# Kernel optimization log

Hardware: AMD Instinct MI355X
Metric: run time of the kernel (lower is better)

## Reference

```python
import jax, jax.numpy as jnp
import numpy as np

N = 25000      # nodes
E = 400000     # edges
IN = 1024      # in_channels
FC = 128       # feature_channels
ADD = 20       # additional_channels
MID = (FC + ADD) // 4   # 37, fc1 output (heads=4)
OUT = 3
EPS = 1e-5
NEG_SLOPE = 0.01


def setup_inputs() -> dict:
    key = jax.random.key(0)
    ks = jax.random.split(key, 16)
    d = {}
    d["features"] = jax.random.normal(ks[0], (N, IN), dtype=jnp.float32)
    d["edges"] = jax.random.randint(ks[1], (2, E), 0, N, dtype=jnp.int64)
    d["edges2"] = jax.random.randint(ks[2], (2, 1000), 0, N, dtype=jnp.int64)
    d["edge_features"] = jax.random.normal(ks[3], (E, 1), dtype=jnp.float32)
    d["additional_feature"] = jax.random.normal(ks[4], (N, ADD), dtype=jnp.float32)
    # SAGEConv params: lin_l (neighbor path, with bias), lin_r (root path, no bias)
    s = 1.0 / np.sqrt(IN)
    d["Wl"] = jax.random.uniform(ks[5], (FC, IN), jnp.float32, -s, s)
    d["bl"] = jax.random.uniform(ks[6], (FC,), jnp.float32, -s, s)
    d["Wr"] = jax.random.uniform(ks[7], (FC, IN), jnp.float32, -s, s)
    s1 = 1.0 / np.sqrt(FC + ADD)
    d["W1"] = jax.random.uniform(ks[8], (MID, FC + ADD), jnp.float32, -s1, s1)
    d["b1"] = jax.random.uniform(ks[9], (MID,), jnp.float32, -s1, s1)
    s2 = 1.0 / np.sqrt(MID)
    d["W2"] = jax.random.uniform(ks[10], (OUT, MID), jnp.float32, -s2, s2)
    d["b2"] = jax.random.uniform(ks[11], (OUT,), jnp.float32, -s2, s2)
    # BatchNorm1d (eval mode -> running stats)
    d["gamma"] = jnp.ones((MID,), jnp.float32)
    d["beta"] = jnp.zeros((MID,), jnp.float32)
    d["run_mean"] = jax.random.normal(ks[12], (MID,), dtype=jnp.float32) * 0.1
    d["run_var"] = jnp.abs(jax.random.normal(ks[13], (MID,), dtype=jnp.float32)) * 0.1 + 1.0
    return d


def reference(features, edges, edges2, edge_features, additional_feature,
              Wl, bl, Wr, W1, b1, W2, b2, gamma, beta, run_mean, run_var):
    src, dst = edges[0], edges[1]  # PyG: messages flow source -> target
    # scatter-mean of neighbor features onto targets
    agg = jax.ops.segment_sum(features[src], dst, num_segments=N)        # [N, IN]
    deg = jax.ops.segment_sum(jnp.ones((E,), features.dtype), dst, num_segments=N)
    agg = agg / jnp.maximum(deg, 1.0)[:, None]
    # SAGEConv: lin_l(mean_neigh) + lin_r(x)
    x = agg @ Wl.T + bl + features @ Wr.T                                 # [N, FC]
    x = jnp.where(x >= 0, x, NEG_SLOPE * x)                               # leaky_relu
    # dropout is identity in eval mode
    x = jnp.concatenate([x, additional_feature], axis=1) @ W1.T + b1      # [N, MID]
    x = jnp.maximum(x, 0.0)                                               # relu
    x = gamma * (x - run_mean) * jax.lax.rsqrt(run_var + EPS) + beta      # BN eval
    return x @ W2.T + b2                                                  # [N, OUT]
```

## Files before the change

### kernel.cpp

```cpp
#include <hip/hip_runtime.h>

#define N_NODES 25000
#define N_EDGES 400000
#define IN_CH 1024
#define FC 128
#define ADD_CH 20
#define XCH 148
#define MID 37
#define OUT_CH 3
#define MAXDEG 64

typedef short bf16x8 __attribute__((ext_vector_type(8)));
typedef float f32x4 __attribute__((ext_vector_type(4)));

__device__ __forceinline__ float bflo(unsigned int v) {
    return __builtin_bit_cast(float, v << 16);
}
__device__ __forceinline__ float bfhi(unsigned int v) {
    return __builtin_bit_cast(float, v & 0xffff0000u);
}
__device__ __forceinline__ unsigned int cvtpk(float a, float b) {
    unsigned int r;
    asm("v_cvt_pk_bf16_f32 %0, %1, %2" : "=v"(r) : "v"(a), "v"(b));
    return r;
}

__device__ __forceinline__ void gload16(const void* g, void* l) {
    __builtin_amdgcn_global_load_lds(
        (const __attribute__((address_space(1))) unsigned int*)g,
        (__attribute__((address_space(3))) unsigned int*)l,
        16, 0, 0);
}

#define WSWZ_B 16
#define ZERO_B 49

__global__ __launch_bounds__(512) void prep(const float* __restrict__ Wl,
                                            const float* __restrict__ Wr,
                                            ushort* __restrict__ Wpk,
                                            int* __restrict__ cursor) {
    int b = blockIdx.x, t = threadIdx.x;
    if (b < WSWZ_B) {
        int w = t >> 6, lane = t & 63, l15 = lane & 15, q8 = (lane >> 4) * 8;
        int ch = b * 16 + l15;
        const float* src = (ch < FC) ? (Wl + (size_t)ch * IN_CH)
                                     : (Wr + (size_t)(ch - FC) * IN_CH);
        #pragma unroll
        for (int j = 0; j < 4; ++j) {
            int kt = w * 4 + j;
            float4 lo = *(const float4*)(src + kt * 32 + q8);
            float4 hi = *(const float4*)(src + kt * 32 + q8 + 4);
            uint4 pk;
            pk.x = cvtpk(lo.x, lo.y); pk.y = cvtpk(lo.z, lo.w);
            pk.z = cvtpk(hi.x, hi.y); pk.w = cvtpk(hi.z, hi.w);
            ((uint4*)Wpk)[((size_t)kt * 16 + b) * 64 + lane] = pk;
        }
    } else {
        int i = (b - WSWZ_B) * 512 + t;
        if (i < N_NODES) cursor[i] = 0;
    }
}

#define GEMM_B 391
#define BUILD_B 782

__global__ __launch_bounds__(512, 4) void gemm_build(const float* __restrict__ A,
                                                     const ushort* __restrict__ Wpk,
                                                     ushort* __restrict__ Py,
                                                     ushort* __restrict__ Pz,
                                                     const int* __restrict__ edges,
                                                     int* __restrict__ cursor,
                                                     int* __restrict__ col) {
    __shared__ uint4 LDS[2][1536];
    int b = blockIdx.x, t = threadIdx.x;
    if (b >= GEMM_B) {
        int e = (b - GEMM_B) * 512 + t;
        if (e < N_EDGES) {
            int dst = edges[N_EDGES + e];
            int pos = atomicAdd(&cursor[dst], 1);
            if (pos < MAXDEG) col[dst * MAXDEG + pos] = edges[e];
        }
        return;
    }
    int m0 = b * 64;

    int ga = t >> 7, hq = (t >> 6) & 1, la = t & 63;
    int nodeA = m0 + ga * 16 + (la & 15);
    if (nodeA >= N_NODES) nodeA = N_NODES - 1;
    const float* Asrc = A + (size_t)nodeA * IN_CH + (la >> 4) * 8 + hq * 4;
    const uint4* Wg = (const uint4*)Wpk;
    int tb = t & ~63;

    int w = t >> 6, lane = t & 63;
    int wm = w >> 2, wn = w & 3;
    int l15 = lane & 15, q = lane >> 4;

    f32x4 acc[4][2] = {};

    gload16(Wg + t,       &LDS[0][tb]);
    gload16(Wg + 512 + t, &LDS[0][512 + tb]);
    gload16(Asrc,         &LDS[0][1024 + tb]);
    __syncthreads();

    for (int c = 0; c < 32; ++c) {
        int cur = c & 1;
        if (c + 1 < 32) {
            const uint4* ws = Wg + (size_t)(c + 1) * 1024;
            gload16(ws + t,       &LDS[cur ^ 1][tb]);
            gload16(ws + 512 + t, &LDS[cur ^ 1][512 + tb]);
            gload16(Asrc + (size_t)(c + 1) * 32, &LDS[cur ^ 1][1024 + tb]);
        }
        bf16x8 wf[4];
        #pragma unroll
        for (int i = 0; i < 4; ++i)
            wf[i] = *(const bf16x8*)&LDS[cur][(wn * 4 + i) * 64 + lane];
        bf16x8 af[2];
        #pragma unroll
        for (int g2 = 0; g2 < 2; ++g2) {
            f32x4 lo = *(const f32x4*)&LDS[cur][1024 + ((wm * 2 + g2) * 2 + 0) * 64 + lane];
            f32x4 hi = *(const f32x4*)&LDS[cur][1024 + ((wm * 2 + g2) * 2 + 1) * 64 + lane];
            uint4 pk;
            pk.x = cvtpk(lo[0], lo[1]); pk.y = cvtpk(lo[2], lo[3]);
            pk.z = cvtpk(hi[0], hi[1]); pk.w = cvtpk(hi[2], hi[3]);
            af[g2] = __builtin_bit_cast(bf16x8, pk);
        }
        #pragma unroll
        for (int i = 0; i < 4; ++i)
            #pragma unroll
            for (int g2 = 0; g2 < 2; ++g2)
                acc[i][g2] = __builtin_amdgcn_mfma_f32_16x16x32_bf16(wf[i], af[g2], acc[i][g2], 0, 0, 0);
        __syncthreads();
    }

    #pragma unroll
    for (int g2 = 0; g2 < 2; ++g2) {
        int node = m0 + wm * 32 + g2 * 16 + l15;
        if (node < N_NODES) {
            ushort* base = (wn < 2) ? (Py + (size_t)node * FC + (wn & 1) * 64 + q * 4)
                                    : (Pz + (size_t)node * FC + (wn & 1) * 64 + q * 4);
            #pragma unroll
            for (int i = 0; i < 4; ++i) {
                f32x4 v = acc[i][g2];
                uint2 pk;
                pk.x = cvtpk(v[0], v[1]);
                pk.y = cvtpk(v[2], v[3]);
                *(uint2*)(base + i * 16) = pk;
            }
        }
    }
}

__global__ __launch_bounds__(512) void fused_tail(const ushort* __restrict__ Py,
                                                  const ushort* __restrict__ Pz,
                                                  const int* __restrict__ deg,
                                                  const int* __restrict__ col,
                                                  const float* __restrict__ addf,
                                                  const float* __restrict__ bl,
                                                  const float* __restrict__ W1,
                                                  const float* __restrict__ b1,
                                                  const float* __restrict__ W2,
                                                  const float* __restrict__ b2,
                                                  const float* __restrict__ gamma,
                                                  const float* __restrict__ beta,
                                                  const float* __restrict__ rmean,
                                                  const float* __restrict__ rvar,
                                                  float* __restrict__ out) {
    __shared__ float W1s[XCH][MID + 3];
    __shared__ float xbuf[8][XCH + 4];
    __shared__ float hbuf[8][MID + 3];
    int t = threadIdx.x;
    for (int idx = t; idx < MID * XCH; idx += 512) {
        int j = idx / XCH, k = idx - j * XCH;
        W1s[k][j] = W1[idx];
    }
    __syncthreads();
    int w = t >> 6, lane = t & 63;
    int n = blockIdx.x * 8 + w;
    bool valid = (n < N_NODES);
    int d = valid ? deg[n] : 0;
    if (d > MAXDEG) d = MAXDEG;
    int g = lane >> 4, c16 = lane & 15;
    float s[8] = {0.f, 0.f, 0.f, 0.f, 0.f, 0.f, 0.f, 0.f};
    if (d > 0) {
        int cidx = col[n * MAXDEG + (lane < d ? lane : 0)];
        for (int i = 0; i < d; i += 16) {
            int e[4];
            uint4 v[4];
            #pragma unroll
            for (int j = 0; j < 4; ++j) {
                int ee = i + g + j * 4;
                e[j] = __shfl(cidx, (ee < d) ? ee : 0);
            }
            #pragma unroll
            for (int j = 0; j < 4; ++j)
                v[j] = *(const uint4*)&Py[(size_t)e[j] * FC + c16 * 8];
            #pragma unroll
            for (int j = 0; j < 4; ++j) {
                if (i + g + j * 4 < d) {
                    s[0] += bflo(v[j].x); s[1] += bfhi(v[j].x);
                    s[2] += bflo(v[j].y); s[3] += bfhi(v[j].y);
                    s[4] += bflo(v[j].z); s[5] += bfhi(v[j].z);
                    s[6] += bflo(v[j].w); s[7] += bfhi(v[j].w);
                }
            }
        }
        #pragma unroll
        for (int r = 0; r < 8; ++r) {
            s[r] += __shfl_xor(s[r], 16);
            s[r] += __shfl_xor(s[r], 32);
        }
    }
    if (valid) {
        if (lane < 16) {
            #pragma unroll
            for (int r = 0; r < 8; ++r) xbuf[w][lane * 8 + r] = s[r];
        }
        float invd = 1.0f / (float)(d > 1 ? d : 1);
        unsigned int vr = *(const unsigned int*)&Pz[(size_t)n * FC + lane * 2];
        float x0 = xbuf[w][2 * lane] * invd + bl[2 * lane] + bflo(vr);
        float x1 = xbuf[w][2 * lane + 1] * invd + bl[2 * lane + 1] + bfhi(vr);
        x0 = (x0 >= 0.f) ? x0 : 0.01f * x0;
        x1 = (x1 >= 0.f) ? x1 : 0.01f * x1;
        xbuf[w][2 * lane] = x0;
        xbuf[w][2 * lane + 1] = x1;
        if (lane < ADD_CH) xbuf[w][FC + lane] = addf[(size_t)n * ADD_CH + lane];
        if (lane < MID) {
            float h = b1[lane];
            #pragma unroll 4
            for (int k = 0; k < XCH; ++k) h += W1s[k][lane] * xbuf[w][k];
            h = fmaxf(h, 0.0f);
            h = gamma[lane] * (h - rmean[lane]) * rsqrtf(rvar[lane] + 1e-5f) + beta[lane];
            hbuf[w][lane] = h;
        }
        if (lane < OUT_CH) {
            float o = b2[lane];
            #pragma unroll
            for (int j = 0; j < MID; ++j) o += W2[lane * MID + j] * hbuf[w][j];
            out[(size_t)n * OUT_CH + lane] = o;
        }
    }
}


extern "C" void kernel_launch(void* const* d_in, const int* in_sizes, int n_in,
                              void* d_out, int out_size, void* d_ws, size_t ws_size,
                              hipStream_t stream) {
    const float* features = (const float*)d_in[0];
    const int*   edges    = (const int*)d_in[1];
    const float* addf     = (const float*)d_in[4];
    const float* Wl       = (const float*)d_in[5];
    const float* bl       = (const float*)d_in[6];
    const float* Wr       = (const float*)d_in[7];
    const float* W1       = (const float*)d_in[8];
    const float* b1       = (const float*)d_in[9];
    const float* W2       = (const float*)d_in[10];
    const float* b2       = (const float*)d_in[11];
    const float* gamma    = (const float*)d_in[12];
    const float* beta     = (const float*)d_in[13];
    const float* rmean    = (const float*)d_in[14];
    const float* rvar     = (const float*)d_in[15];
    float* out = (float*)d_out;

    char* ws = (char*)d_ws;
    size_t off = 0;
    ushort* Py = (ushort*)(ws + off);     off += (size_t)N_NODES * FC * 2;
    ushort* Pz = (ushort*)(ws + off);     off += (size_t)N_NODES * FC * 2;
    ushort* Wpk = (ushort*)(ws + off);    off += (size_t)32 * 16 * 64 * 16;
    int* cursor = (int*)(ws + off);       off += (size_t)N_NODES * 4;
    int* col = (int*)(ws + off);          off += (size_t)N_NODES * MAXDEG * 4;

    prep<<<WSWZ_B + ZERO_B, 512, 0, stream>>>(Wl, Wr, Wpk, cursor);

    gemm_build<<<GEMM_B + BUILD_B, 512, 0, stream>>>(features, Wpk, Py, Pz,
                                                     edges, cursor, col);

    fused_tail<<<(N_NODES + 7) / 8, 512, 0, stream>>>(Py, Pz, cursor, col, addf, bl,
                                                      W1, b1, W2, b2, gamma, beta,
                                                      rmean, rvar, out);
}
```

Baseline: 268.4 us.

## Halve GEMM row tile to 32 nodes and double block count

Result: slower. 279.6 us (+4.2%).

```diff
diff --git a/kernel.cpp b/kernel.cpp
--- a/kernel.cpp
+++ b/kernel.cpp
@@ -61,17 +61,17 @@
     }
 }
 
-#define GEMM_B 391
+#define GEMM_B 782
 #define BUILD_B 782
 
-__global__ __launch_bounds__(512, 4) void gemm_build(const float* __restrict__ A,
+__global__ __launch_bounds__(512, 8) void gemm_build(const float* __restrict__ A,
                                                      const ushort* __restrict__ Wpk,
                                                      ushort* __restrict__ Py,
                                                      ushort* __restrict__ Pz,
                                                      const int* __restrict__ edges,
                                                      int* __restrict__ cursor,
                                                      int* __restrict__ col) {
-    __shared__ uint4 LDS[2][1536];
+    __shared__ uint4 LDS[2][1280];
     int b = blockIdx.x, t = threadIdx.x;
     if (b >= GEMM_B) {
         int e = (b - GEMM_B) * 512 + t;
@@ -82,24 +82,22 @@
         }
         return;
     }
-    int m0 = b * 64;
-
-    int ga = t >> 7, hq = (t >> 6) & 1, la = t & 63;
-    int nodeA = m0 + ga * 16 + (la & 15);
+    int m0 = b * 32;
+    int w = t >> 6, lane = t & 63;
+    int l15 = lane & 15, q = lane >> 4;
+    int tb = t & ~63;
+
+    int ga = (t >> 7) & 1, hq = (t >> 6) & 1;
+    int nodeA = m0 + ga * 16 + l15;
     if (nodeA >= N_NODES) nodeA = N_NODES - 1;
-    const float* Asrc = A + (size_t)nodeA * IN_CH + (la >> 4) * 8 + hq * 4;
+    const float* Asrc = A + (size_t)nodeA * IN_CH + q * 8 + hq * 4;
     const uint4* Wg = (const uint4*)Wpk;
-    int tb = t & ~63;
-
-    int w = t >> 6, lane = t & 63;
-    int wm = w >> 2, wn = w & 3;
-    int l15 = lane & 15, q = lane >> 4;
-
-    f32x4 acc[4][2] = {};
+
+    f32x4 acc[2][2] = {};
 
     gload16(Wg + t,       &LDS[0][tb]);
     gload16(Wg + 512 + t, &LDS[0][512 + tb]);
-    gload16(Asrc,         &LDS[0][1024 + tb]);
+    if (w < 4) gload16(Asrc, &LDS[0][1024 + tb]);
     __syncthreads();
 
     for (int c = 0; c < 32; ++c) {
@@ -108,43 +106,37 @@
             const uint4* ws = Wg + (size_t)(c + 1) * 1024;
             gload16(ws + t,       &LDS[cur ^ 1][tb]);
             gload16(ws + 512 + t, &LDS[cur ^ 1][512 + tb]);
-            gload16(Asrc + (size_t)(c + 1) * 32, &LDS[cur ^ 1][1024 + tb]);
-        }
-        bf16x8 wf[4];
-        #pragma unroll
-        for (int i = 0; i < 4; ++i)
-            wf[i] = *(const bf16x8*)&LDS[cur][(wn * 4 + i) * 64 + lane];
-        bf16x8 af[2];
+            if (w < 4) gload16(Asrc + (size_t)(c + 1) * 32, &LDS[cur ^ 1][1024 + tb]);
+        }
+        bf16x8 wf0 = *(const bf16x8*)&LDS[cur][(w * 2 + 0) * 64 + lane];
+        bf16x8 wf1 = *(const bf16x8*)&LDS[cur][(w * 2 + 1) * 64 + lane];
         #pragma unroll
         for (int g2 = 0; g2 < 2; ++g2) {
-            f32x4 lo = *(const f32x4*)&LDS[cur][1024 + ((wm * 2 + g2) * 2 + 0) * 64 + lane];
-            f32x4 hi = *(const f32x4*)&LDS[cur][1024 + ((wm * 2 + g2) * 2 + 1) * 64 + lane];
+            f32x4 lo = *(const f32x4*)&LDS[cur][1024 + (g2 * 2 + 0) * 64 + lane];
+            f32x4 hi = *(const f32x4*)&LDS[cur][1024 + (g2 * 2 + 1) * 64 + lane];
             uint4 pk;
             pk.x = cvtpk(lo[0], lo[1]); pk.y = cvtpk(lo[2], lo[3]);
             pk.z = cvtpk(hi[0], hi[1]); pk.w = cvtpk(hi[2], hi[3]);
-            af[g2] = __builtin_bit_cast(bf16x8, pk);
-        }
-        #pragma unroll
-        for (int i = 0; i < 4; ++i)
-            #pragma unroll
-            for (int g2 = 0; g2 < 2; ++g2)
-                acc[i][g2] = __builtin_amdgcn_mfma_f32_16x16x32_bf16(wf[i], af[g2], acc[i][g2], 0, 0, 0);
+            bf16x8 af = __builtin_bit_cast(bf16x8, pk);
+            acc[0][g2] = __builtin_amdgcn_mfma_f32_16x16x32_bf16(wf0, af, acc[0][g2], 0, 0, 0);
+            acc[1][g2] = __builtin_amdgcn_mfma_f32_16x16x32_bf16(wf1, af, acc[1][g2], 0, 0, 0);
+        }
         __syncthreads();
     }
 
     #pragma unroll
     for (int g2 = 0; g2 < 2; ++g2) {
-        int node = m0 + wm * 32 + g2 * 16 + l15;
+        int node = m0 + g2 * 16 + l15;
         if (node < N_NODES) {
-            ushort* base = (wn < 2) ? (Py + (size_t)node * FC + (wn & 1) * 64 + q * 4)
-                                    : (Pz + (size_t)node * FC + (wn & 1) * 64 + q * 4);
-            #pragma unroll
-            for (int i = 0; i < 4; ++i) {
-                f32x4 v = acc[i][g2];
+            ushort* base = (w < 4) ? (Py + (size_t)node * FC + w * 32)
+                                   : (Pz + (size_t)node * FC + (w - 4) * 32);
+            #pragma unroll
+            for (int cf = 0; cf < 2; ++cf) {
+                f32x4 v = acc[cf][g2];
                 uint2 pk;
                 pk.x = cvtpk(v[0], v[1]);
                 pk.y = cvtpk(v[2], v[3]);
-                *(uint2*)(base + i * 16) = pk;
+                *(uint2*)(base + cf * 16 + q * 4) = pk;
             }
         }
     }
```

## Replace LDS-staged GEMM with register-prefetched direct loads; pad degree counters

Applied to the files above, without the earlier changes.

Result: slower. 319.4 us (+19.0%).

```diff
diff --git a/kernel.cpp b/kernel.cpp
--- a/kernel.cpp
+++ b/kernel.cpp
@@ -9,6 +9,7 @@
 #define MID 37
 #define OUT_CH 3
 #define MAXDEG 64
+#define CSTRIDE 16
 
 typedef short bf16x8 __attribute__((ext_vector_type(8)));
 typedef float f32x4 __attribute__((ext_vector_type(4)));
@@ -23,13 +24,6 @@
     unsigned int r;
     asm("v_cvt_pk_bf16_f32 %0, %1, %2" : "=v"(r) : "v"(a), "v"(b));
     return r;
-}
-
-__device__ __forceinline__ void gload16(const void* g, void* l) {
-    __builtin_amdgcn_global_load_lds(
-        (const __attribute__((address_space(1))) unsigned int*)g,
-        (__attribute__((address_space(3))) unsigned int*)l,
-        16, 0, 0);
 }
 
 #define WSWZ_B 16
@@ -57,87 +51,108 @@
         }
     } else {
         int i = (b - WSWZ_B) * 512 + t;
-        if (i < N_NODES) cursor[i] = 0;
-    }
-}
-
-#define GEMM_B 391
-#define BUILD_B 782
-
-__global__ __launch_bounds__(512, 4) void gemm_build(const float* __restrict__ A,
+        if (i < N_NODES) {
+            uint4 z = {0, 0, 0, 0};
+            uint4* dst = (uint4*)(cursor + (size_t)i * CSTRIDE);
+            dst[0] = z; dst[1] = z; dst[2] = z; dst[3] = z;
+        }
+    }
+}
+
+#define GEMM_B 782
+#define BUILD_B 391
+
+__global__ __launch_bounds__(256, 4) void gemm_build(const float* __restrict__ A,
                                                      const ushort* __restrict__ Wpk,
                                                      ushort* __restrict__ Py,
                                                      ushort* __restrict__ Pz,
                                                      const int* __restrict__ edges,
                                                      int* __restrict__ cursor,
                                                      int* __restrict__ col) {
-    __shared__ uint4 LDS[2][1536];
     int b = blockIdx.x, t = threadIdx.x;
     if (b >= GEMM_B) {
-        int e = (b - GEMM_B) * 512 + t;
-        if (e < N_EDGES) {
-            int dst = edges[N_EDGES + e];
-            int pos = atomicAdd(&cursor[dst], 1);
-            if (pos < MAXDEG) col[dst * MAXDEG + pos] = edges[e];
+        int base = (b - GEMM_B) * 1024 + t;
+        int src[4], dst[4], pos[4];
+        #pragma unroll
+        for (int k = 0; k < 4; ++k) {
+            int e = base + k * 256;
+            bool v = (e < N_EDGES);
+            dst[k] = v ? edges[N_EDGES + e] : 0;
+            src[k] = v ? edges[e] : 0;
+        }
+        #pragma unroll
+        for (int k = 0; k < 4; ++k) {
+            int e = base + k * 256;
+            if (e < N_EDGES)
+                pos[k] = atomicAdd(&cursor[(size_t)dst[k] * CSTRIDE], 1);
+        }
+        #pragma unroll
+        for (int k = 0; k < 4; ++k) {
+            int e = base + k * 256;
+            if (e < N_EDGES && pos[k] < MAXDEG)
+                col[dst[k] * MAXDEG + pos[k]] = src[k];
         }
         return;
     }
-    int m0 = b * 64;
-
-    int ga = t >> 7, hq = (t >> 6) & 1, la = t & 63;
-    int nodeA = m0 + ga * 16 + (la & 15);
-    if (nodeA >= N_NODES) nodeA = N_NODES - 1;
-    const float* Asrc = A + (size_t)nodeA * IN_CH + (la >> 4) * 8 + hq * 4;
-    const uint4* Wg = (const uint4*)Wpk;
-    int tb = t & ~63;
-
+    int m0 = b * 32;
     int w = t >> 6, lane = t & 63;
-    int wm = w >> 2, wn = w & 3;
     int l15 = lane & 15, q = lane >> 4;
 
+    int n0 = m0 + l15;      if (n0 >= N_NODES) n0 = N_NODES - 1;
+    int n1 = m0 + 16 + l15; if (n1 >= N_NODES) n1 = N_NODES - 1;
+    const float* A0 = A + (size_t)n0 * IN_CH + q * 8;
+    const float* A1 = A + (size_t)n1 * IN_CH + q * 8;
+    const uint4* Wld = (const uint4*)Wpk + (size_t)(w * 4) * 64 + lane;
+
     f32x4 acc[4][2] = {};
 
-    gload16(Wg + t,       &LDS[0][tb]);
-    gload16(Wg + 512 + t, &LDS[0][512 + tb]);
-    gload16(Asrc,         &LDS[0][1024 + tb]);
-    __syncthreads();
-
-    for (int c = 0; c < 32; ++c) {
-        int cur = c & 1;
-        if (c + 1 < 32) {
-            const uint4* ws = Wg + (size_t)(c + 1) * 1024;
-            gload16(ws + t,       &LDS[cur ^ 1][tb]);
-            gload16(ws + 512 + t, &LDS[cur ^ 1][512 + tb]);
-            gload16(Asrc + (size_t)(c + 1) * 32, &LDS[cur ^ 1][1024 + tb]);
-        }
-        bf16x8 wf[4];
-        #pragma unroll
-        for (int i = 0; i < 4; ++i)
-            wf[i] = *(const bf16x8*)&LDS[cur][(wn * 4 + i) * 64 + lane];
-        bf16x8 af[2];
-        #pragma unroll
-        for (int g2 = 0; g2 < 2; ++g2) {
-            f32x4 lo = *(const f32x4*)&LDS[cur][1024 + ((wm * 2 + g2) * 2 + 0) * 64 + lane];
-            f32x4 hi = *(const f32x4*)&LDS[cur][1024 + ((wm * 2 + g2) * 2 + 1) * 64 + lane];
-            uint4 pk;
-            pk.x = cvtpk(lo[0], lo[1]); pk.y = cvtpk(lo[2], lo[3]);
-            pk.z = cvtpk(hi[0], hi[1]); pk.w = cvtpk(hi[2], hi[3]);
-            af[g2] = __builtin_bit_cast(bf16x8, pk);
-        }
-        #pragma unroll
-        for (int i = 0; i < 4; ++i)
-            #pragma unroll
-            for (int g2 = 0; g2 < 2; ++g2)
-                acc[i][g2] = __builtin_amdgcn_mfma_f32_16x16x32_bf16(wf[i], af[g2], acc[i][g2], 0, 0, 0);
-        __syncthreads();
-    }
+    uint4 wq0, wq1, wq2, wq3;
+    f32x4 aq0, aq1, aq2, aq3;
+    #define LDW(kt) { const uint4* p = Wld + (size_t)(kt) * 1024;                  \
+                      wq0 = p[0]; wq1 = p[64]; wq2 = p[128]; wq3 = p[192]; }
+    #define LDA(kt) { aq0 = *(const f32x4*)(A0 + (kt) * 32);                       \
+                      aq1 = *(const f32x4*)(A0 + (kt) * 32 + 4);                   \
+                      aq2 = *(const f32x4*)(A1 + (kt) * 32);                       \
+                      aq3 = *(const f32x4*)(A1 + (kt) * 32 + 4); }
+    LDW(0)
+    LDA(0)
+    #pragma unroll
+    for (int kt = 0; kt < 32; ++kt) {
+        uint4 wc0 = wq0, wc1 = wq1, wc2 = wq2, wc3 = wq3;
+        f32x4 ac0 = aq0, ac1 = aq1, ac2 = aq2, ac3 = aq3;
+        if (kt + 1 < 32) {
+            LDW(kt + 1)
+            LDA(kt + 1)
+        }
+        uint4 p0, p1;
+        p0.x = cvtpk(ac0[0], ac0[1]); p0.y = cvtpk(ac0[2], ac0[3]);
+        p0.z = cvtpk(ac1[0], ac1[1]); p0.w = cvtpk(ac1[2], ac1[3]);
+        p1.x = cvtpk(ac2[0], ac2[1]); p1.y = cvtpk(ac2[2], ac2[3]);
+        p1.z = cvtpk(ac3[0], ac3[1]); p1.w = cvtpk(ac3[2], ac3[3]);
+        bf16x8 af0 = __builtin_bit_cast(bf16x8, p0);
+        bf16x8 af1 = __builtin_bit_cast(bf16x8, p1);
+        bf16x8 wf0 = __builtin_bit_cast(bf16x8, wc0);
+        bf16x8 wf1 = __builtin_bit_cast(bf16x8, wc1);
+        bf16x8 wf2 = __builtin_bit_cast(bf16x8, wc2);
+        bf16x8 wf3 = __builtin_bit_cast(bf16x8, wc3);
+        acc[0][0] = __builtin_amdgcn_mfma_f32_16x16x32_bf16(wf0, af0, acc[0][0], 0, 0, 0);
+        acc[0][1] = __builtin_amdgcn_mfma_f32_16x16x32_bf16(wf0, af1, acc[0][1], 0, 0, 0);
+        acc[1][0] = __builtin_amdgcn_mfma_f32_16x16x32_bf16(wf1, af0, acc[1][0], 0, 0, 0);
+        acc[1][1] = __builtin_amdgcn_mfma_f32_16x16x32_bf16(wf1, af1, acc[1][1], 0, 0, 0);
+        acc[2][0] = __builtin_amdgcn_mfma_f32_16x16x32_bf16(wf2, af0, acc[2][0], 0, 0, 0);
+        acc[2][1] = __builtin_amdgcn_mfma_f32_16x16x32_bf16(wf2, af1, acc[2][1], 0, 0, 0);
+        acc[3][0] = __builtin_amdgcn_mfma_f32_16x16x32_bf16(wf3, af0, acc[3][0], 0, 0, 0);
+        acc[3][1] = __builtin_amdgcn_mfma_f32_16x16x32_bf16(wf3, af1, acc[3][1], 0, 0, 0);
+    }
+    #undef LDW
+    #undef LDA
 
     #pragma unroll
     for (int g2 = 0; g2 < 2; ++g2) {
-        int node = m0 + wm * 32 + g2 * 16 + l15;
+        int node = m0 + g2 * 16 + l15;
         if (node < N_NODES) {
-            ushort* base = (wn < 2) ? (Py + (size_t)node * FC + (wn & 1) * 64 + q * 4)
-                                    : (Pz + (size_t)node * FC + (wn & 1) * 64 + q * 4);
+            ushort* base = (w < 2) ? (Py + (size_t)node * FC + (w & 1) * 64 + q * 4)
+                                   : (Pz + (size_t)node * FC + (w & 1) * 64 + q * 4);
             #pragma unroll
             for (int i = 0; i < 4; ++i) {
                 f32x4 v = acc[i][g2];
@@ -177,7 +192,7 @@
     int w = t >> 6, lane = t & 63;
     int n = blockIdx.x * 8 + w;
     bool valid = (n < N_NODES);
-    int d = valid ? deg[n] : 0;
+    int d = valid ? deg[(size_t)n * CSTRIDE] : 0;
     if (d > MAXDEG) d = MAXDEG;
     int g = lane >> 4, c16 = lane & 15;
     float s[8] = {0.f, 0.f, 0.f, 0.f, 0.f, 0.f, 0.f, 0.f};
@@ -266,12 +281,12 @@
     ushort* Py = (ushort*)(ws + off);     off += (size_t)N_NODES * FC * 2;
     ushort* Pz = (ushort*)(ws + off);     off += (size_t)N_NODES * FC * 2;
     ushort* Wpk = (ushort*)(ws + off);    off += (size_t)32 * 16 * 64 * 16;
-    int* cursor = (int*)(ws + off);       off += (size_t)N_NODES * 4;
+    int* cursor = (int*)(ws + off);       off += (size_t)N_NODES * CSTRIDE * 4;
     int* col = (int*)(ws + off);          off += (size_t)N_NODES * MAXDEG * 4;
 
     prep<<<WSWZ_B + ZERO_B, 512, 0, stream>>>(Wl, Wr, Wpk, cursor);
 
-    gemm_build<<<GEMM_B + BUILD_B, 512, 0, stream>>>(features, Wpk, Py, Pz,
+    gemm_build<<<GEMM_B + BUILD_B, 256, 0, stream>>>(features, Wpk, Py, Pz,
                                                      edges, cursor, col);
 
     fused_tail<<<(N_NODES + 7) / 8, 512, 0, stream>>>(Py, Pz, cursor, col, addf, bl,
```
